# Performance work log

Hardware: AMD Instinct MI355X
Metric: run time of the kernel (lower is better)

Reference implementation:

```python
import jax, jax.numpy as jnp
import numpy as np

B, S, E, H = 2, 2048, 1024, 16
D = E // H


def setup_inputs() -> dict:
    key = jax.random.key(0)
    ks = jax.random.split(key, 12)
    init = lambda k, shp: (jax.random.normal(k, shp, dtype=jnp.float32) * 0.02)
    return {
        "q": jax.random.normal(ks[0], (B, S, E), dtype=jnp.float32),
        "k": jax.random.normal(ks[1], (B, S, E), dtype=jnp.float32),
        "v": jax.random.normal(ks[2], (B, S, E), dtype=jnp.float32),
        "wq": init(ks[3], (E, E)), "bq": jnp.zeros((E,), jnp.float32),
        "wk": init(ks[4], (E, E)), "bk": jnp.zeros((E,), jnp.float32),
        "wv": init(ks[5], (E, E)), "bv": jnp.zeros((E,), jnp.float32),
        "wo": init(ks[6], (E, E)), "bo": jnp.zeros((E,), jnp.float32),
        "gamma": jnp.ones((E,), jnp.float32),
        "beta": jnp.zeros((E,), jnp.float32),
        "mask": 1,
    }


def _split_heads(x):
    # [B,S,E] -> [B,H,S,D]
    return x.reshape(x.shape[0], x.shape[1], H, D).transpose(0, 2, 1, 3)


def _mha(q, k, v, wq, bq, wk, bk, wv, bv, wo, bo, gamma, beta, causal):
    residual = q
    query = _split_heads(q @ wq + bq)
    key = _split_heads(k @ wk + bk)
    value = _split_heads(v @ wv + bv)
    scale = jnp.sqrt(jnp.float32(D)) + 1e-8  # matches torch: sqrt(dk) + 1e-8
    score = jnp.einsum("bhqd,bhkd->bhqk", query, key) / scale
    if causal:
        cm = jnp.tril(jnp.ones((S, S), dtype=bool))  # 1 - triu(...,1)
        score = jnp.where(cm[None, None], score, -jnp.inf)
    attn = jax.nn.softmax(score, axis=-1)
    ctx = jnp.einsum("bhqk,bhkd->bhqd", attn, value)
    ctx = ctx.transpose(0, 2, 1, 3).reshape(ctx.shape[0], S, E)
    o = ctx @ wo + bo  # dropout is identity in eval mode
    x = residual + o
    mu = jnp.mean(x, axis=-1, keepdims=True)
    var = jnp.var(x, axis=-1, keepdims=True)
    return (x - mu) / jnp.sqrt(var + 1e-5) * gamma + beta


def reference(q, k, v, wq, bq, wk, bk, wv, bv, wo, bo, gamma, beta, mask):
    return _mha(q, k, v, wq, bq, wk, bk, wv, bv, wo, bo, gamma, beta, bool(mask))
```

## Files before the change

### kernel.cpp

```cpp
#include <hip/hip_runtime.h>
#include <hip/hip_bf16.h>

typedef __bf16 bf16x8 __attribute__((ext_vector_type(8)));
typedef __attribute__((ext_vector_type(8))) short short8_t;
typedef __attribute__((ext_vector_type(4))) short short4_t;
typedef __attribute__((ext_vector_type(4))) float f32x4;

#define DEV __device__ __forceinline__

constexpr int Bc = 2, Sc = 2048, Ec = 1024, Hc = 16, Dc = 64;
constexpr int Mc = Bc * Sc;
constexpr int NT = Sc / 64;
constexpr float kQS = (float)((1.0 / (8.0 + 1e-8)) * 1.4426950408889634);

DEV short f2bf(float f) {
  unsigned int u = __builtin_bit_cast(unsigned int, f);
  unsigned int r = u + 0x7fffu + ((u >> 16) & 1u);
  return (short)(r >> 16);
}
DEV short bfc(float f) { __bf16 h = (__bf16)f; return __builtin_bit_cast(short, h); }

DEV float fexp2(float x) {
#if __has_builtin(__builtin_amdgcn_exp2f)
  return __builtin_amdgcn_exp2f(x);
#else
  float r;
  asm("v_exp_f32 %0, %1" : "=v"(r) : "v"(x));
  return r;
#endif
}

DEV void gload16(const short* g, short* lds) {
  __builtin_amdgcn_global_load_lds((const __attribute__((address_space(1))) void*)g,
                                   (__attribute__((address_space(3))) void*)lds, 16, 0, 0);
}

struct Prep {
  const float* w[4]; short* wt[4];
  const float* x[3]; short* y[3];
};
__global__ __launch_bounds__(256) void k_prep(Prep a) {
  const int bid = blockIdx.x;
  if (bid < 4096) {
    __shared__ float tile[32][33];
    const int z = bid >> 10, bk = (bid >> 5) & 31, bn = bid & 31;
    const float* w = a.w[z];
    short* wt = a.wt[z];
    int tx = threadIdx.x & 31, ty = threadIdx.x >> 5;
#pragma unroll
    for (int i = 0; i < 4; i++)
      tile[ty + i * 8][tx] = w[(size_t)(bk * 32 + ty + i * 8) * Ec + bn * 32 + tx];
    __syncthreads();
#pragma unroll
    for (int i = 0; i < 4; i++)
      wt[(size_t)(bn * 32 + ty + i * 8) * Ec + bk * 32 + tx] = f2bf(tile[tx][ty + i * 8]);
  } else {
    const int idx = bid - 4096;
    const int z = idx >> 11, c = idx & 2047;
    const float* x = a.x[z];
    short* y = a.y[z];
    size_t i = ((size_t)c * 256 + threadIdx.x) * 8;
    float4 v0 = *(const float4*)(x + i);
    float4 v1 = *(const float4*)(x + i + 4);
    short8_t h;
    h[0] = bfc(v0.x); h[1] = bfc(v0.y); h[2] = bfc(v0.z); h[3] = bfc(v0.w);
    h[4] = bfc(v1.x); h[5] = bfc(v1.y); h[6] = bfc(v1.z); h[7] = bfc(v1.w);
    *(short8_t*)(y + i) = h;
  }
}

DEV void gemm_mfma(const short* lA, const short* lB, f32x4 (&acc)[4][4], int lane, int wm, int wn) {
#pragma unroll
  for (int kc = 0; kc < 2; kc++) {
    bf16x8 a[4], b[4];
#pragma unroll
    for (int mf = 0; mf < 4; mf++) {
      int row = wm * 64 + mf * 16 + (lane & 15);
      int ch = (kc * 4 + (lane >> 4)) ^ (row & 7);
      a[mf] = *(const bf16x8*)&lA[row * 64 + (ch << 3)];
    }
#pragma unroll
    for (int nf = 0; nf < 4; nf++) {
      int row = wn * 64 + nf * 16 + (lane & 15);
      int ch = (kc * 4 + (lane >> 4)) ^ (row & 7);
      b[nf] = *(const bf16x8*)&lB[row * 64 + (ch << 3)];
    }
#pragma unroll
    for (int mf = 0; mf < 4; mf++)
#pragma unroll
      for (int nf = 0; nf < 4; nf++)
        acc[mf][nf] = __builtin_amdgcn_mfma_f32_16x16x32_bf16(a[mf], b[nf], acc[mf][nf], 0, 0, 0);
  }
}

struct QKV3 { const short* A[3]; const short* Bt[3]; const float* bias[3]; short* out[3]; };

__global__ __launch_bounds__(256, 2) void k_gemm_qkv(QKV3 args) {
  __shared__ short lA[2][128 * 64];
  __shared__ short lB[2][128 * 64];
  int lin = blockIdx.x + 8 * blockIdx.y + 256 * blockIdx.z;
  lin = (lin & 7) * 96 + (lin >> 3);
  const int bx = lin & 7, by = (lin >> 3) & 31, z = lin >> 8;
  const short* A = args.A[z];
  const short* Bt = args.Bt[z];
  const float* bias = args.bias[z];
  short* out = args.out[z];
  const int t = threadIdx.x;
  const int m0 = by * 128, n0 = bx * 128;
  const int lane = t & 63, wid = t >> 6;
  const int wm = wid >> 1, wn = wid & 1;
  const int rl = lane >> 3, chs = ((lane & 7) ^ rl) << 3;

  f32x4 acc[4][4];
#pragma unroll
  for (int i = 0; i < 4; i++)
#pragma unroll
    for (int j = 0; j < 4; j++) acc[i][j] = {0.f, 0.f, 0.f, 0.f};

  auto stage = [&](int st, int buf) {
    const int k0 = st * 64;
#pragma unroll
    for (int j = 0; j < 4; j++) {
      int r0 = wid * 32 + j * 8;
      gload16(A + (size_t)(m0 + r0 + rl) * Ec + k0 + chs, &lA[buf][r0 * 64]);
      gload16(Bt + (size_t)(n0 + r0 + rl) * Ec + k0 + chs, &lB[buf][r0 * 64]);
    }
  };
  stage(0, 0);
  stage(1, 1);
  for (int s = 0; s < 15; s++) {
    asm volatile("s_waitcnt vmcnt(8)" ::: "memory");
    __builtin_amdgcn_s_barrier();
    gemm_mfma(lA[s & 1], lB[s & 1], acc, lane, wm, wn);
    __builtin_amdgcn_s_barrier();
    if (s + 2 < 16) stage(s + 2, s & 1);
  }
  asm volatile("s_waitcnt vmcnt(0)" ::: "memory");
  __builtin_amdgcn_s_barrier();
  gemm_mfma(lA[1], lB[1], acc, lane, wm, wn);

#pragma unroll
  for (int mf = 0; mf < 4; mf++) {
#pragma unroll
    for (int nf = 0; nf < 4; nf++) {
      int col = n0 + wn * 64 + nf * 16 + (lane & 15);
      float bs = bias[col];
      int row0 = m0 + wm * 64 + mf * 16 + ((lane >> 4) << 2);
      int bh = ((row0 >> 11) << 4) + (col >> 6);
      int d = col & 63;
      size_t bhbase = (size_t)bh * Sc * Dc;
      if (z == 0) {
#pragma unroll
        for (int r = 0; r < 4; r++) {
          int row = row0 + r;
          size_t off = bhbase + (size_t)(row & 2047) * Dc + d;
          out[off] = f2bf((acc[mf][nf][r] + bs) * kQS);
        }
      } else if (z == 1) {
#pragma unroll
        for (int r = 0; r < 4; r++) {
          int sr = (row0 + r) & 2047;
          size_t off = bhbase + (size_t)(sr >> 4) * 1024 + ((d >> 5) * 512) +
                       (((d >> 3) & 3) * 128) + ((sr & 15) * 8) + (d & 7);
          out[off] = f2bf(acc[mf][nf][r] + bs);
        }
      } else {
        short4_t h;
#pragma unroll
        for (int r = 0; r < 4; r++) h[r] = f2bf(acc[mf][nf][r] + bs);
        int s0 = row0 & 2047;
        size_t off = bhbase + (size_t)(s0 >> 6) * 4096 + (((s0 >> 5) & 1) * 2048) +
                     (((d >> 4) & 3) * 512) + ((((s0 >> 3) & 3) * 16 + (d & 15)) * 8) + (s0 & 7);
        *(short4_t*)&out[off] = h;
      }
    }
  }
}

__global__ __launch_bounds__(256, 2) void k_gemm_o(const short* __restrict__ A,
                                                   const short* __restrict__ Bt,
                                                   const float* __restrict__ bias,
                                                   const float* __restrict__ res,
                                                   float* __restrict__ out) {
  __shared__ short lA[2][128 * 64];
  __shared__ short lB[2][128 * 64];
  int lin = blockIdx.x + 8 * blockIdx.y;
  lin = (lin & 7) * 32 + (lin >> 3);
  const int bx = lin & 7, by = lin >> 3;
  const int t = threadIdx.x;
  const int m0 = by * 128, n0 = bx * 128;
  const int lane = t & 63, wid = t >> 6;
  const int wm = wid >> 1, wn = wid & 1;
  const int rl = lane >> 3, chs = ((lane & 7) ^ rl) << 3;

  f32x4 acc[4][4];
#pragma unroll
  for (int i = 0; i < 4; i++)
#pragma unroll
    for (int j = 0; j < 4; j++) acc[i][j] = {0.f, 0.f, 0.f, 0.f};

  auto stage = [&](int st, int buf) {
    const int k0 = st * 64;
#pragma unroll
    for (int j = 0; j < 4; j++) {
      int r0 = wid * 32 + j * 8;
      gload16(A + (size_t)(m0 + r0 + rl) * Ec + k0 + chs, &lA[buf][r0 * 64]);
      gload16(Bt + (size_t)(n0 + r0 + rl) * Ec + k0 + chs, &lB[buf][r0 * 64]);
    }
  };
  stage(0, 0);
  stage(1, 1);
  for (int s = 0; s < 15; s++) {
    asm volatile("s_waitcnt vmcnt(8)" ::: "memory");
    __builtin_amdgcn_s_barrier();
    gemm_mfma(lA[s & 1], lB[s & 1], acc, lane, wm, wn);
    __builtin_amdgcn_s_barrier();
    if (s + 2 < 16) stage(s + 2, s & 1);
  }
  asm volatile("s_waitcnt vmcnt(0)" ::: "memory");
  __builtin_amdgcn_s_barrier();
  gemm_mfma(lA[1], lB[1], acc, lane, wm, wn);

#pragma unroll
  for (int mf = 0; mf < 4; mf++) {
#pragma unroll
    for (int nf = 0; nf < 4; nf++) {
      int col = n0 + wn * 64 + nf * 16 + (lane & 15);
      float bs = bias[col];
#pragma unroll
      for (int r = 0; r < 4; r++) {
        int row = m0 + wm * 64 + mf * 16 + ((lane >> 4) << 2) + r;
        out[(size_t)row * Ec + col] = acc[mf][nf][r] + bs + res[(size_t)row * Ec + col];
      }
    }
  }
}

__global__ __launch_bounds__(256, 3) void k_attn7(const short* __restrict__ Qp,
                                                  const short* __restrict__ Kf,
                                                  const short* __restrict__ Vf,
                                                  const int* __restrict__ maskp,
                                                  short* __restrict__ ctx) {
  __shared__ short lP[64 * 64];
  const int lin = blockIdx.x;
  const int bh = lin & 31;
  const int qtord = lin >> 5;
  const int qt = (qtord & 8) ? (qtord ^ 7) : qtord;
  const int t = threadIdx.x, lane = t & 63, w = t >> 6;
  const int gs = lane >> 4, l15 = lane & 15;
  const bool causal = maskp[0] != 0;
  const int b = bh >> 4, h = bh & 15;
  const size_t base = (size_t)bh * Sc * Dc;
  const int ktend = causal ? qt : (NT - 1);

  bf16x8 aq[2];
  {
    const short* qptr = Qp + base + (size_t)(qt * 64 + w * 16 + l15) * Dc + gs * 8;
    aq[0] = *(const bf16x8*)(qptr);
    aq[1] = *(const bf16x8*)(qptr + 32);
  }
  bf16x8 ones;
#pragma unroll
  for (int j = 0; j < 8; j++) ones[j] = (__bf16)1.0f;

  f32x4 oacc[4], lsum;
#pragma unroll
  for (int i = 0; i < 4; i++) oacc[i] = {0.f, 0.f, 0.f, 0.f};
  lsum = {0.f, 0.f, 0.f, 0.f};

  const int prow = w * 16 + l15, pswz = l15 & 7;
  short* pw[4];
  const short* pr[2];
#pragma unroll
  for (int mf = 0; mf < 4; mf++)
    pw[mf] = &lP[prow * 64 + (((2 * mf + (gs >> 1)) ^ pswz) << 3) + (gs & 1) * 4];
#pragma unroll
  for (int kc = 0; kc < 2; kc++)
    pr[kc] = &lP[prow * 64 + (((kc * 4 + gs) ^ pswz) << 3)];

  const short* Kb = Kf + base + lane * 8;
  const short* Vb = Vf + base + lane * 8;
  const int qloc = w * 16 + l15;

  bf16x8 kA[2][4], kB[2][4];
  {
#pragma unroll
    for (int mf = 0; mf < 4; mf++) {
      kA[0][mf] = *(const bf16x8*)(Kb + mf * 1024);
      kA[1][mf] = *(const bf16x8*)(Kb + mf * 1024 + 512);
    }
  }

  int kt = 0;
  auto body = [&](bf16x8 (&kc_)[2][4], bf16x8 (&kn_)[2][4]) {
    if (kt < ktend) {
      const short* kp = Kb + (kt + 1) * 4096;
#pragma unroll
      for (int mf = 0; mf < 4; mf++) {
        kn_[0][mf] = *(const bf16x8*)(kp + mf * 1024);
        kn_[1][mf] = *(const bf16x8*)(kp + mf * 1024 + 512);
      }
    }
    const short* vp = Vb + kt * 4096;
    bf16x8 vf[2][4];
#pragma unroll
    for (int c2 = 0; c2 < 2; c2++)
#pragma unroll
      for (int df = 0; df < 4; df++)
        vf[c2][df] = *(const bf16x8*)(vp + c2 * 2048 + df * 512);
    __builtin_amdgcn_sched_barrier(0);

    f32x4 s[4];
#pragma unroll
    for (int mf = 0; mf < 4; mf++) s[mf] = {0.f, 0.f, 0.f, 0.f};
#pragma unroll
    for (int c2 = 0; c2 < 2; c2++)
#pragma unroll
      for (int mf = 0; mf < 4; mf++)
        s[mf] = __builtin_amdgcn_mfma_f32_16x16x32_bf16(kc_[c2][mf], aq[c2], s[mf], 0, 0, 0);

    if (causal && kt == qt) {
#pragma unroll
      for (int mf = 0; mf < 4; mf++) {
        short4_t hh;
#pragma unroll
        for (int r = 0; r < 4; r++) {
          float p = fexp2(s[mf][r]);
          if ((mf * 16 + gs * 4 + r) > qloc) p = 0.f;
          hh[r] = bfc(p);
        }
        *(short4_t*)pw[mf] = hh;
      }
    } else {
#pragma unroll
      for (int mf = 0; mf < 4; mf++) {
        short4_t hh;
#pragma unroll
        for (int r = 0; r < 4; r++) hh[r] = bfc(fexp2(s[mf][r]));
        *(short4_t*)pw[mf] = hh;
      }
    }

    bf16x8 pa[2];
    pa[0] = *(const bf16x8*)pr[0];
    pa[1] = *(const bf16x8*)pr[1];
#pragma unroll
    for (int c2 = 0; c2 < 2; c2++) {
      lsum = __builtin_amdgcn_mfma_f32_16x16x32_bf16(pa[c2], ones, lsum, 0, 0, 0);
#pragma unroll
      for (int df = 0; df < 4; df++)
        oacc[df] = __builtin_amdgcn_mfma_f32_16x16x32_bf16(pa[c2], vf[c2][df], oacc[df], 0, 0, 0);
    }
  };

  while (true) {
    body(kA, kB);
    if (++kt > ktend) break;
    body(kB, kA);
    if (++kt > ktend) break;
  }

#pragma unroll
  for (int r = 0; r < 4; r++) {
    float ib = 1.0f / lsum[r];
    int sr = qt * 64 + w * 16 + (gs << 2) + r;
#pragma unroll
    for (int df = 0; df < 4; df++) {
      int col = h * 64 + df * 16 + l15;
      ctx[(size_t)(b * Sc + sr) * Ec + col] = f2bf(oacc[df][r] * ib);
    }
  }
}

__global__ __launch_bounds__(256) void k_ln(float* __restrict__ x,
                                            const float* __restrict__ gamma,
                                            const float* __restrict__ beta) {
  int row = blockIdx.x, t = threadIdx.x;
  float4 v = *(const float4*)(x + (size_t)row * Ec + t * 4);
  float s = v.x + v.y + v.z + v.w;
  float sq = v.x * v.x + v.y * v.y + v.z * v.z + v.w * v.w;
#pragma unroll
  for (int m = 1; m < 64; m <<= 1) {
    s += __shfl_xor(s, m);
    sq += __shfl_xor(sq, m);
  }
  __shared__ float red[8];
  if ((t & 63) == 0) {
    red[t >> 6] = s;
    red[4 + (t >> 6)] = sq;
  }
  __syncthreads();
  s = red[0] + red[1] + red[2] + red[3];
  sq = red[4] + red[5] + red[6] + red[7];
  float mu = s * (1.f / Ec);
  float var = sq * (1.f / Ec) - mu * mu;
  float rstd = rsqrtf(var + 1e-5f);
  float4 g = *(const float4*)(gamma + t * 4);
  float4 bb = *(const float4*)(beta + t * 4);
  v.x = (v.x - mu) * rstd * g.x + bb.x;
  v.y = (v.y - mu) * rstd * g.y + bb.y;
  v.z = (v.z - mu) * rstd * g.z + bb.z;
  v.w = (v.w - mu) * rstd * g.w + bb.w;
  *(float4*)(x + (size_t)row * Ec + t * 4) = v;
}

extern "C" void kernel_launch(void* const* d_in, const int* in_sizes, int n_in,
                              void* d_out, int out_size, void* d_ws, size_t ws_size,
                              hipStream_t stream) {
  const float* q = (const float*)d_in[0];
  const float* k = (const float*)d_in[1];
  const float* v = (const float*)d_in[2];
  const float* wq = (const float*)d_in[3];
  const float* bq = (const float*)d_in[4];
  const float* wk = (const float*)d_in[5];
  const float* bk = (const float*)d_in[6];
  const float* wv = (const float*)d_in[7];
  const float* bv = (const float*)d_in[8];
  const float* wo = (const float*)d_in[9];
  const float* bo = (const float*)d_in[10];
  const float* gamma = (const float*)d_in[11];
  const float* beta = (const float*)d_in[12];
  const int* maskp = (const int*)d_in[13];
  float* out = (float*)d_out;

  short* wtq = (short*)d_ws;
  short* wtk = wtq + (size_t)Ec * Ec;
  short* wtv = wtk + (size_t)Ec * Ec;
  short* wto = wtv + (size_t)Ec * Ec;
  short* Qp = wto + (size_t)Ec * Ec;
  short* Kf = Qp + (size_t)Mc * Ec;
  short* Vf = Kf + (size_t)Mc * Ec;
  short* ctx = Vf + (size_t)Mc * Ec;

  short* xq = (short*)d_out;
  short* xk = xq + (size_t)Mc * Ec;
  short* xv = ctx;

  dim3 tb(256);

  Prep pargs;
  pargs.w[0] = wq; pargs.w[1] = wk; pargs.w[2] = wv; pargs.w[3] = wo;
  pargs.wt[0] = wtq; pargs.wt[1] = wtk; pargs.wt[2] = wtv; pargs.wt[3] = wto;
  pargs.x[0] = q; pargs.x[1] = k; pargs.x[2] = v;
  pargs.y[0] = xq; pargs.y[1] = xk; pargs.y[2] = xv;
  k_prep<<<dim3(4096 + 3 * (Mc * Ec / 2048)), tb, 0, stream>>>(pargs);

  QKV3 gargs;
  gargs.A[0] = xq; gargs.A[1] = xk; gargs.A[2] = xv;
  gargs.Bt[0] = wtq; gargs.Bt[1] = wtk; gargs.Bt[2] = wtv;
  gargs.bias[0] = bq; gargs.bias[1] = bk; gargs.bias[2] = bv;
  gargs.out[0] = Qp; gargs.out[1] = Kf; gargs.out[2] = Vf;
  k_gemm_qkv<<<dim3(Ec / 128, Mc / 128, 3), tb, 0, stream>>>(gargs);

  k_attn7<<<dim3(NT * Bc * Hc), tb, 0, stream>>>(Qp, Kf, Vf, maskp, ctx);

  k_gemm_o<<<dim3(Ec / 128, Mc / 128), tb, 0, stream>>>(ctx, wto, bo, q, out);

  k_ln<<<dim3(Mc), tb, 0, stream>>>(out, gamma, beta);
}
```

Baseline: 119.7 us.

## Fuse fp32-to-bf16 activation conversion into QKV GEMM A-tile loading

Removes the separate activation-conversion pass from the prep kernel. The QKV GEMM now reads fp32 q/k/v directly into registers, converts them to bf16 and writes swizzled LDS tiles, with software pipelining across stages. B tiles still use direct global-to-LDS loads. It also raises wave priority around the MFMA blocks in the attention kernel. This saves a full write and re-read of the bf16 activations, but doubles the A-side global read bytes per tile and adds register pressure and VALU conversion work inside the GEMM loop.

After: 149.3 us. 1.25x slower.

```diff
diff --git a/kernel.cpp b/kernel.cpp
--- a/kernel.cpp
+++ b/kernel.cpp
@@ -35,38 +35,21 @@
                                    (__attribute__((address_space(3))) void*)lds, 16, 0, 0);
 }
 
-struct Prep {
-  const float* w[4]; short* wt[4];
-  const float* x[3]; short* y[3];
-};
+struct Prep { const float* w[4]; short* wt[4]; };
 __global__ __launch_bounds__(256) void k_prep(Prep a) {
+  __shared__ float tile[32][33];
   const int bid = blockIdx.x;
-  if (bid < 4096) {
-    __shared__ float tile[32][33];
-    const int z = bid >> 10, bk = (bid >> 5) & 31, bn = bid & 31;
-    const float* w = a.w[z];
-    short* wt = a.wt[z];
-    int tx = threadIdx.x & 31, ty = threadIdx.x >> 5;
-#pragma unroll
-    for (int i = 0; i < 4; i++)
-      tile[ty + i * 8][tx] = w[(size_t)(bk * 32 + ty + i * 8) * Ec + bn * 32 + tx];
-    __syncthreads();
-#pragma unroll
-    for (int i = 0; i < 4; i++)
-      wt[(size_t)(bn * 32 + ty + i * 8) * Ec + bk * 32 + tx] = f2bf(tile[tx][ty + i * 8]);
-  } else {
-    const int idx = bid - 4096;
-    const int z = idx >> 11, c = idx & 2047;
-    const float* x = a.x[z];
-    short* y = a.y[z];
-    size_t i = ((size_t)c * 256 + threadIdx.x) * 8;
-    float4 v0 = *(const float4*)(x + i);
-    float4 v1 = *(const float4*)(x + i + 4);
-    short8_t h;
-    h[0] = bfc(v0.x); h[1] = bfc(v0.y); h[2] = bfc(v0.z); h[3] = bfc(v0.w);
-    h[4] = bfc(v1.x); h[5] = bfc(v1.y); h[6] = bfc(v1.z); h[7] = bfc(v1.w);
-    *(short8_t*)(y + i) = h;
-  }
+  const int z = bid >> 10, bk = (bid >> 5) & 31, bn = bid & 31;
+  const float* w = a.w[z];
+  short* wt = a.wt[z];
+  int tx = threadIdx.x & 31, ty = threadIdx.x >> 5;
+#pragma unroll
+  for (int i = 0; i < 4; i++)
+    tile[ty + i * 8][tx] = w[(size_t)(bk * 32 + ty + i * 8) * Ec + bn * 32 + tx];
+  __syncthreads();
+#pragma unroll
+  for (int i = 0; i < 4; i++)
+    wt[(size_t)(bn * 32 + ty + i * 8) * Ec + bk * 32 + tx] = f2bf(tile[tx][ty + i * 8]);
 }
 
 DEV void gemm_mfma(const short* lA, const short* lB, f32x4 (&acc)[4][4], int lane, int wm, int wn) {
@@ -93,7 +76,7 @@
   }
 }
 
-struct QKV3 { const short* A[3]; const short* Bt[3]; const float* bias[3]; short* out[3]; };
+struct QKV3 { const float* A[3]; const short* Bt[3]; const float* bias[3]; short* out[3]; };
 
 __global__ __launch_bounds__(256, 2) void k_gemm_qkv(QKV3 args) {
   __shared__ short lA[2][128 * 64];
@@ -101,7 +84,7 @@
   int lin = blockIdx.x + 8 * blockIdx.y + 256 * blockIdx.z;
   lin = (lin & 7) * 96 + (lin >> 3);
   const int bx = lin & 7, by = (lin >> 3) & 31, z = lin >> 8;
-  const short* A = args.A[z];
+  const float* A = args.A[z];
   const short* Bt = args.Bt[z];
   const float* bias = args.bias[z];
   short* out = args.out[z];
@@ -110,6 +93,8 @@
   const int lane = t & 63, wid = t >> 6;
   const int wm = wid >> 1, wn = wid & 1;
   const int rl = lane >> 3, chs = ((lane & 7) ^ rl) << 3;
+  const int arow = t >> 1, ahalf = t & 1, aswz = arow & 7;
+  const float* Arow = A + (size_t)(m0 + arow) * Ec + ahalf * 32;
 
   f32x4 acc[4][4];
 #pragma unroll
@@ -117,27 +102,56 @@
 #pragma unroll
     for (int j = 0; j < 4; j++) acc[i][j] = {0.f, 0.f, 0.f, 0.f};
 
-  auto stage = [&](int st, int buf) {
+  float4 rA[8];
+  auto loadA = [&](int st) {
+    const float* ap = Arow + st * 64;
+#pragma unroll
+    for (int j = 0; j < 8; j++) rA[j] = *(const float4*)(ap + j * 4);
+  };
+  auto writeA = [&](int st) {
+    short* aw = &lA[st & 1][arow * 64];
+#pragma unroll
+    for (int j = 0; j < 4; j++) {
+      short8_t h;
+      h[0] = bfc(rA[2 * j].x); h[1] = bfc(rA[2 * j].y);
+      h[2] = bfc(rA[2 * j].z); h[3] = bfc(rA[2 * j].w);
+      h[4] = bfc(rA[2 * j + 1].x); h[5] = bfc(rA[2 * j + 1].y);
+      h[6] = bfc(rA[2 * j + 1].z); h[7] = bfc(rA[2 * j + 1].w);
+      *(short8_t*)&aw[((ahalf * 4 + j) ^ aswz) << 3] = h;
+    }
+  };
+  auto stageB = [&](int st, int buf) {
     const int k0 = st * 64;
 #pragma unroll
     for (int j = 0; j < 4; j++) {
       int r0 = wid * 32 + j * 8;
-      gload16(A + (size_t)(m0 + r0 + rl) * Ec + k0 + chs, &lA[buf][r0 * 64]);
       gload16(Bt + (size_t)(n0 + r0 + rl) * Ec + k0 + chs, &lB[buf][r0 * 64]);
     }
   };
-  stage(0, 0);
-  stage(1, 1);
-  for (int s = 0; s < 15; s++) {
-    asm volatile("s_waitcnt vmcnt(8)" ::: "memory");
-    __builtin_amdgcn_s_barrier();
+
+  stageB(0, 0);
+  stageB(1, 1);
+  __builtin_amdgcn_sched_barrier(0);
+  loadA(0);
+  __builtin_amdgcn_sched_barrier(0);
+  writeA(0);
+  loadA(1);
+  asm volatile("s_waitcnt lgkmcnt(0)" ::: "memory");
+  __builtin_amdgcn_s_barrier();
+
+  for (int s = 0; s < 16; s++) {
     gemm_mfma(lA[s & 1], lB[s & 1], acc, lane, wm, wn);
     __builtin_amdgcn_s_barrier();
-    if (s + 2 < 16) stage(s + 2, s & 1);
-  }
-  asm volatile("s_waitcnt vmcnt(0)" ::: "memory");
-  __builtin_amdgcn_s_barrier();
-  gemm_mfma(lA[1], lB[1], acc, lane, wm, wn);
+    if (s < 15) writeA(s + 1);
+    if (s + 2 < 16) {
+      stageB(s + 2, s & 1);
+      __builtin_amdgcn_sched_barrier(0);
+      loadA(s + 2);
+      __builtin_amdgcn_sched_barrier(0);
+    }
+    asm volatile("s_waitcnt lgkmcnt(0)" ::: "memory");
+    __builtin_amdgcn_s_barrier();
+  }
 
 #pragma unroll
   for (int mf = 0; mf < 4; mf++) {
@@ -313,11 +327,13 @@
     f32x4 s[4];
 #pragma unroll
     for (int mf = 0; mf < 4; mf++) s[mf] = {0.f, 0.f, 0.f, 0.f};
+    __builtin_amdgcn_s_setprio(1);
 #pragma unroll
     for (int c2 = 0; c2 < 2; c2++)
 #pragma unroll
       for (int mf = 0; mf < 4; mf++)
         s[mf] = __builtin_amdgcn_mfma_f32_16x16x32_bf16(kc_[c2][mf], aq[c2], s[mf], 0, 0, 0);
+    __builtin_amdgcn_s_setprio(0);
 
     if (causal && kt == qt) {
 #pragma unroll
@@ -344,6 +360,7 @@
     bf16x8 pa[2];
     pa[0] = *(const bf16x8*)pr[0];
     pa[1] = *(const bf16x8*)pr[1];
+    __builtin_amdgcn_s_setprio(1);
 #pragma unroll
     for (int c2 = 0; c2 < 2; c2++) {
       lsum = __builtin_amdgcn_mfma_f32_16x16x32_bf16(pa[c2], ones, lsum, 0, 0, 0);
@@ -351,6 +368,7 @@
       for (int df = 0; df < 4; df++)
         oacc[df] = __builtin_amdgcn_mfma_f32_16x16x32_bf16(pa[c2], vf[c2][df], oacc[df], 0, 0, 0);
     }
+    __builtin_amdgcn_s_setprio(0);
   };
 
   while (true) {
@@ -432,21 +450,15 @@
   short* Vf = Kf + (size_t)Mc * Ec;
   short* ctx = Vf + (size_t)Mc * Ec;
 
-  short* xq = (short*)d_out;
-  short* xk = xq + (size_t)Mc * Ec;
-  short* xv = ctx;
-
   dim3 tb(256);
 
   Prep pargs;
   pargs.w[0] = wq; pargs.w[1] = wk; pargs.w[2] = wv; pargs.w[3] = wo;
   pargs.wt[0] = wtq; pargs.wt[1] = wtk; pargs.wt[2] = wtv; pargs.wt[3] = wto;
-  pargs.x[0] = q; pargs.x[1] = k; pargs.x[2] = v;
-  pargs.y[0] = xq; pargs.y[1] = xk; pargs.y[2] = xv;
-  k_prep<<<dim3(4096 + 3 * (Mc * Ec / 2048)), tb, 0, stream>>>(pargs);
+  k_prep<<<dim3(4096), tb, 0, stream>>>(pargs);
 
   QKV3 gargs;
-  gargs.A[0] = xq; gargs.A[1] = xk; gargs.A[2] = xv;
+  gargs.A[0] = q; gargs.A[1] = k; gargs.A[2] = v;
   gargs.Bt[0] = wtq; gargs.Bt[1] = wtk; gargs.Bt[2] = wtv;
   gargs.bias[0] = bq; gargs.bias[1] = bk; gargs.bias[2] = bv;
   gargs.out[0] = Qp; gargs.out[1] = Kf; gargs.out[2] = Vf;
```

## Pair complementary causal query tiles per block to balance work and share K/V

Applied to the files above, without the earlier changes.

Each attention block now processes two query tiles, qi and NT-1-qi, so every block does the same amount of causal work. Each K/V tile it loads is reused for both query tiles. This halves the grid and removes the tail imbalance from uneven causal rows. It also adds s_setprio around the MFMA sections and lowers the occupancy hint from 3 to 2 to make room for the doubled accumulator registers, which leaves fewer waves to hide latency.

Measured after the change: 116.3 us. 1.03x faster.

```diff
diff --git a/kernel.cpp b/kernel.cpp
--- a/kernel.cpp
+++ b/kernel.cpp
@@ -236,37 +236,43 @@
   }
 }
 
-__global__ __launch_bounds__(256, 3) void k_attn7(const short* __restrict__ Qp,
+__global__ __launch_bounds__(256, 2) void k_attn8(const short* __restrict__ Qp,
                                                   const short* __restrict__ Kf,
                                                   const short* __restrict__ Vf,
                                                   const int* __restrict__ maskp,
                                                   short* __restrict__ ctx) {
   __shared__ short lP[64 * 64];
   const int lin = blockIdx.x;
-  const int bh = lin & 31;
-  const int qtord = lin >> 5;
-  const int qt = (qtord & 8) ? (qtord ^ 7) : qtord;
+  const int bh = lin & 31, qi = lin >> 5;
+  const int qtA = qi, qtB = NT - 1 - qi;
   const int t = threadIdx.x, lane = t & 63, w = t >> 6;
   const int gs = lane >> 4, l15 = lane & 15;
   const bool causal = maskp[0] != 0;
   const int b = bh >> 4, h = bh & 15;
   const size_t base = (size_t)bh * Sc * Dc;
-  const int ktend = causal ? qt : (NT - 1);
-
-  bf16x8 aq[2];
+  const int ktend = causal ? qtB : (NT - 1);
+
+  bf16x8 aqA[2], aqB[2];
   {
-    const short* qptr = Qp + base + (size_t)(qt * 64 + w * 16 + l15) * Dc + gs * 8;
-    aq[0] = *(const bf16x8*)(qptr);
-    aq[1] = *(const bf16x8*)(qptr + 32);
+    const short* qpA = Qp + base + (size_t)(qtA * 64 + w * 16 + l15) * Dc + gs * 8;
+    const short* qpB = Qp + base + (size_t)(qtB * 64 + w * 16 + l15) * Dc + gs * 8;
+    aqA[0] = *(const bf16x8*)(qpA);
+    aqA[1] = *(const bf16x8*)(qpA + 32);
+    aqB[0] = *(const bf16x8*)(qpB);
+    aqB[1] = *(const bf16x8*)(qpB + 32);
   }
   bf16x8 ones;
 #pragma unroll
   for (int j = 0; j < 8; j++) ones[j] = (__bf16)1.0f;
 
-  f32x4 oacc[4], lsum;
-#pragma unroll
-  for (int i = 0; i < 4; i++) oacc[i] = {0.f, 0.f, 0.f, 0.f};
-  lsum = {0.f, 0.f, 0.f, 0.f};
+  f32x4 oA[4], oB[4], lsA, lsB;
+#pragma unroll
+  for (int i = 0; i < 4; i++) {
+    oA[i] = {0.f, 0.f, 0.f, 0.f};
+    oB[i] = {0.f, 0.f, 0.f, 0.f};
+  }
+  lsA = {0.f, 0.f, 0.f, 0.f};
+  lsB = {0.f, 0.f, 0.f, 0.f};
 
   const int prow = w * 16 + l15, pswz = l15 & 7;
   short* pw[4];
@@ -283,43 +289,26 @@
   const int qloc = w * 16 + l15;
 
   bf16x8 kA[2][4], kB[2][4];
-  {
-#pragma unroll
-    for (int mf = 0; mf < 4; mf++) {
-      kA[0][mf] = *(const bf16x8*)(Kb + mf * 1024);
-      kA[1][mf] = *(const bf16x8*)(Kb + mf * 1024 + 512);
-    }
+#pragma unroll
+  for (int mf = 0; mf < 4; mf++) {
+    kA[0][mf] = *(const bf16x8*)(Kb + mf * 1024);
+    kA[1][mf] = *(const bf16x8*)(Kb + mf * 1024 + 512);
   }
 
   int kt = 0;
-  auto body = [&](bf16x8 (&kc_)[2][4], bf16x8 (&kn_)[2][4]) {
-    if (kt < ktend) {
-      const short* kp = Kb + (kt + 1) * 4096;
-#pragma unroll
-      for (int mf = 0; mf < 4; mf++) {
-        kn_[0][mf] = *(const bf16x8*)(kp + mf * 1024);
-        kn_[1][mf] = *(const bf16x8*)(kp + mf * 1024 + 512);
-      }
-    }
-    const short* vp = Vb + kt * 4096;
-    bf16x8 vf[2][4];
-#pragma unroll
-    for (int c2 = 0; c2 < 2; c2++)
-#pragma unroll
-      for (int df = 0; df < 4; df++)
-        vf[c2][df] = *(const bf16x8*)(vp + c2 * 2048 + df * 512);
-    __builtin_amdgcn_sched_barrier(0);
-
+  auto tilepass = [&](const bf16x8 (&kc_)[2][4], const bf16x8 (&vf)[2][4],
+                      const bf16x8 (&aq)[2], f32x4 (&oacc)[4], f32x4& lsum, bool diag) {
     f32x4 s[4];
 #pragma unroll
     for (int mf = 0; mf < 4; mf++) s[mf] = {0.f, 0.f, 0.f, 0.f};
+    __builtin_amdgcn_s_setprio(1);
 #pragma unroll
     for (int c2 = 0; c2 < 2; c2++)
 #pragma unroll
       for (int mf = 0; mf < 4; mf++)
         s[mf] = __builtin_amdgcn_mfma_f32_16x16x32_bf16(kc_[c2][mf], aq[c2], s[mf], 0, 0, 0);
-
-    if (causal && kt == qt) {
+    __builtin_amdgcn_s_setprio(0);
+    if (diag) {
 #pragma unroll
       for (int mf = 0; mf < 4; mf++) {
         short4_t hh;
@@ -340,10 +329,10 @@
         *(short4_t*)pw[mf] = hh;
       }
     }
-
     bf16x8 pa[2];
     pa[0] = *(const bf16x8*)pr[0];
     pa[1] = *(const bf16x8*)pr[1];
+    __builtin_amdgcn_s_setprio(1);
 #pragma unroll
     for (int c2 = 0; c2 < 2; c2++) {
       lsum = __builtin_amdgcn_mfma_f32_16x16x32_bf16(pa[c2], ones, lsum, 0, 0, 0);
@@ -351,6 +340,30 @@
       for (int df = 0; df < 4; df++)
         oacc[df] = __builtin_amdgcn_mfma_f32_16x16x32_bf16(pa[c2], vf[c2][df], oacc[df], 0, 0, 0);
     }
+    __builtin_amdgcn_s_setprio(0);
+  };
+
+  auto body = [&](bf16x8 (&kc_)[2][4], bf16x8 (&kn_)[2][4]) {
+    if (kt < ktend) {
+      const short* kp = Kb + (kt + 1) * 4096;
+#pragma unroll
+      for (int mf = 0; mf < 4; mf++) {
+        kn_[0][mf] = *(const bf16x8*)(kp + mf * 1024);
+        kn_[1][mf] = *(const bf16x8*)(kp + mf * 1024 + 512);
+      }
+    }
+    const short* vp = Vb + kt * 4096;
+    bf16x8 vf[2][4];
+#pragma unroll
+    for (int c2 = 0; c2 < 2; c2++)
+#pragma unroll
+      for (int df = 0; df < 4; df++)
+        vf[c2][df] = *(const bf16x8*)(vp + c2 * 2048 + df * 512);
+    __builtin_amdgcn_sched_barrier(0);
+
+    tilepass(kc_, vf, aqB, oB, lsB, causal && (kt == qtB));
+    if (!causal || (kt <= qtA))
+      tilepass(kc_, vf, aqA, oA, lsA, causal && (kt == qtA));
   };
 
   while (true) {
@@ -362,12 +375,15 @@
 
 #pragma unroll
   for (int r = 0; r < 4; r++) {
-    float ib = 1.0f / lsum[r];
-    int sr = qt * 64 + w * 16 + (gs << 2) + r;
+    float ibB = 1.0f / lsB[r];
+    float ibA = 1.0f / lsA[r];
+    int srB = qtB * 64 + w * 16 + (gs << 2) + r;
+    int srA = qtA * 64 + w * 16 + (gs << 2) + r;
 #pragma unroll
     for (int df = 0; df < 4; df++) {
       int col = h * 64 + df * 16 + l15;
-      ctx[(size_t)(b * Sc + sr) * Ec + col] = f2bf(oacc[df][r] * ib);
+      ctx[(size_t)(b * Sc + srB) * Ec + col] = f2bf(oB[df][r] * ibB);
+      ctx[(size_t)(b * Sc + srA) * Ec + col] = f2bf(oA[df][r] * ibA);
     }
   }
 }
@@ -452,7 +468,7 @@
   gargs.out[0] = Qp; gargs.out[1] = Kf; gargs.out[2] = Vf;
   k_gemm_qkv<<<dim3(Ec / 128, Mc / 128, 3), tb, 0, stream>>>(gargs);
 
-  k_attn7<<<dim3(NT * Bc * Hc), tb, 0, stream>>>(Qp, Kf, Vf, maskp, ctx);
+  k_attn8<<<dim3(NT / 2 * Bc * Hc), tb, 0, stream>>>(Qp, Kf, Vf, maskp, ctx);
 
   k_gemm_o<<<dim3(Ec / 128, Mc / 128), tb, 0, stream>>>(ctx, wto, bo, q, out);
 
```
